# Kernel optimization log

Hardware: AMD Instinct MI355X
Metric: run time of the kernel (lower is better)

## Reference

```python
import jax, jax.numpy as jnp
import numpy as np

B, S, DIM = 2, 2048, 2048
H = 16
Q_RANK, KV_RANK = 512, 512
D_NOPE, D_ROPE, D_V = 128, 64, 128
D_QK = D_NOPE + D_ROPE  # 192
EPS = 1e-6
SCALE = D_QK ** -0.5


def setup_inputs() -> dict:
    key = jax.random.key(0)
    ks = jax.random.split(key, 8)
    x = jax.random.normal(ks[0], (B, S, DIM), dtype=jnp.float32)
    # real RoPE table: theta_i = 10000^{-2i/d}, angles = pos * theta
    inv_freq = 1.0 / (10000.0 ** (np.arange(0, D_ROPE, 2, dtype=np.float32) / D_ROPE))
    ang = np.arange(S, dtype=np.float32)[:, None] * inv_freq[None, :]  # (S, D_ROPE//2)
    freqs_cis = jnp.asarray(np.stack([np.cos(ang), np.sin(ang)], axis=-1))  # (S, 32, 2)
    std = 0.02
    wq_a = jax.random.normal(ks[1], (Q_RANK, DIM), dtype=jnp.float32) * std
    wq_b = jax.random.normal(ks[2], (H * D_QK, Q_RANK), dtype=jnp.float32) * std
    wkv_a = jax.random.normal(ks[3], (KV_RANK + D_ROPE, DIM), dtype=jnp.float32) * std
    wkv_b = jax.random.normal(ks[4], (H * (D_NOPE + D_V), KV_RANK), dtype=jnp.float32) * std
    wo = jax.random.normal(ks[5], (DIM, H * D_V), dtype=jnp.float32) * std
    q_norm_w = jnp.ones((Q_RANK,), dtype=jnp.float32)
    kv_norm_w = jnp.ones((KV_RANK,), dtype=jnp.float32)
    return {"x": x, "freqs_cis": freqs_cis, "wq_a": wq_a, "wq_b": wq_b,
            "q_norm_w": q_norm_w, "wkv_a": wkv_a, "kv_norm_w": kv_norm_w,
            "wkv_b": wkv_b, "wo": wo}


def _rmsnorm(x, w):
    var = jnp.mean(jnp.square(x), axis=-1, keepdims=True)
    return x * jax.lax.rsqrt(var + EPS) * w


def _rope(x, freqs_cis):
    # x: (B, S, h, d); freqs_cis: (S, d//2, 2) as (cos, sin). Pairs are interleaved (x0,x1),(x2,x3),...
    xr, xi = x[..., 0::2], x[..., 1::2]
    cos = freqs_cis[None, :, None, :, 0]
    sin = freqs_cis[None, :, None, :, 1]
    yr = xr * cos - xi * sin
    yi = xr * sin + xi * cos
    return jnp.stack([yr, yi], axis=-1).reshape(x.shape)


def reference(x, freqs_cis, wq_a, wq_b, q_norm_w, wkv_a, kv_norm_w, wkv_b, wo):
    b, s, _ = x.shape
    # low-rank Q projection: wq_a -> RMSNorm -> wq_b
    q = _rmsnorm(x @ wq_a.T, q_norm_w) @ wq_b.T
    q = q.reshape(b, s, H, D_QK)
    q_nope, q_pe = q[..., :D_NOPE], q[..., D_NOPE:]
    q = jnp.concatenate([q_nope, _rope(q_pe, freqs_cis)], axis=-1)  # (b,s,H,192)
    # KV path
    kv = x @ wkv_a.T  # (b,s,KV_RANK+D_ROPE)
    kv_lat, k_pe = kv[..., :KV_RANK], kv[..., KV_RANK:]
    k_pe = _rope(k_pe[:, :, None, :], freqs_cis)  # (b,s,1,64)
    kv = (_rmsnorm(kv_lat, kv_norm_w) @ wkv_b.T).reshape(b, s, H, D_NOPE + D_V)
    k_nope, v = kv[..., :D_NOPE], kv[..., D_NOPE:]
    k = jnp.concatenate([k_nope, jnp.broadcast_to(k_pe, (b, s, H, D_ROPE))], axis=-1)
    # causal scaled-dot-product attention
    scores = jnp.einsum('bshd,bthd->bhst', q, k) * SCALE
    mask = jnp.tril(jnp.ones((s, s), dtype=bool))
    scores = jnp.where(mask[None, None], scores, jnp.finfo(scores.dtype).min)
    probs = jax.nn.softmax(scores, axis=-1)
    out = jnp.einsum('bhst,bthd->bshd', probs, v).reshape(b, s, H * D_V)
    return out @ wo.T
```

## Files before the change

### kernel.cpp

```cpp
#include <hip/hip_runtime.h>
#include <cstdint>
#include <cstddef>


typedef unsigned short u16;
typedef unsigned int u32;
typedef unsigned long long u64;
typedef __attribute__((ext_vector_type(8))) short bf16x8;
typedef __attribute__((ext_vector_type(4))) float floatx4;

#define MFMA16x16x32 __builtin_amdgcn_mfma_f32_16x16x32_bf16

#define QSCALE 0.10411755f
#define THR_L2 11.541560f

__device__ __forceinline__ u16 f2bf(float f) {
  u32 u = __float_as_uint(f);
  u32 r = (u + 0x7fffu + ((u >> 16) & 1u)) >> 16;
  return (u16)r;
}
__device__ __forceinline__ float bf2f(u16 b) {
  return __uint_as_float(((u32)b) << 16);
}
__device__ __forceinline__ u32 cvtpk(float lo, float hi) {
  u32 r;
  asm("v_cvt_pk_bf16_f32 %0, %1, %2" : "=v"(r) : "v"(lo), "v"(hi));
  return r;
}
__device__ __forceinline__ void gload16(const void* g, void* l) {
  __builtin_amdgcn_global_load_lds(
      (const __attribute__((address_space(1))) void*)g,
      (__attribute__((address_space(3))) void*)l, 16, 0, 0);
}

__global__ __launch_bounds__(256) void cvt_all(
    const float* __restrict__ s0, const float* __restrict__ s1,
    const float* __restrict__ s2, const float* __restrict__ s3,
    const float* __restrict__ s4, const float* __restrict__ s5,
    u16* __restrict__ d0, u16* __restrict__ d1, u16* __restrict__ d2,
    u16* __restrict__ d3, u16* __restrict__ d4, u16* __restrict__ d5) {
  constexpr int ST1 = 2097152;
  constexpr int ST2 = ST1 + 262144;
  constexpr int ST3 = ST2 + 294912;
  constexpr int ST4 = ST3 + 393216;
  constexpr int ST5 = ST4 + 524288;
  constexpr int TOT = ST5 + 1048576;
  int i = blockIdx.x * 256 + threadIdx.x;
  int stride = gridDim.x * 256;
  for (; i < TOT; i += stride) {
    const float* sp;
    u16* dp;
    int j;
    if (i < ST1)      { sp = s0; dp = d0; j = i; }
    else if (i < ST2) { sp = s1; dp = d1; j = i - ST1; }
    else if (i < ST3) { sp = s2; dp = d2; j = i - ST2; }
    else if (i < ST4) { sp = s3; dp = d3; j = i - ST3; }
    else if (i < ST5) { sp = s4; dp = d4; j = i - ST4; }
    else              { sp = s5; dp = d5; j = i - ST5; }
    float4 v = ((const float4*)sp)[j];
    ushort4 o;
    o.x = f2bf(v.x); o.y = f2bf(v.y); o.z = f2bf(v.z); o.w = f2bf(v.w);
    ((ushort4*)dp)[j] = o;
  }
}

template <int BM, int BN, int EPI>
__global__ __launch_bounds__(512) void gemm8(const u16* __restrict__ A,
                                             const u16* __restrict__ B,
                                             void* __restrict__ Cv,
                                             int M, int N, int K,
                                             const float* __restrict__ fcp,
                                             void* __restrict__ aux) {
  constexpr int WM = BM / 2;
  constexpr int AF = WM / 16;
  constexpr int WN = BN / 4;
  constexpr int FN = WN / 16;
  constexpr int LA = BM * 4 / 512;
  constexpr int LB = BN * 4 / 512;
  constexpr int S = LA + LB;
  __shared__ alignas(16) u16 As[2][BM * 32];
  __shared__ alignas(16) u16 Bs[2][BN * 32];
  const int m0 = blockIdx.y * BM, n0 = blockIdx.x * BN;
  const int t = threadIdx.x;
  const int wv = t >> 6, lane = t & 63, g = lane >> 4, qq = lane & 15;
  const int wr = wv >> 2, wc = wv & 3;
  const int fsw = (qq >> 1) & 3;
  size_t aoff[LA], boff[LB];
#pragma unroll
  for (int i = 0; i < LA; ++i) {
    int seg = t + i * 512;
    int row = seg >> 2, sl = seg & 3;
    aoff[i] = (size_t)(m0 + row) * K + (sl ^ ((row >> 1) & 3)) * 8;
  }
#pragma unroll
  for (int i = 0; i < LB; ++i) {
    int seg = t + i * 512;
    int row = seg >> 2, sl = seg & 3;
    boff[i] = (size_t)(n0 + row) * K + (sl ^ ((row >> 1) & 3)) * 8;
  }
  const floatx4 fz = {0.f, 0.f, 0.f, 0.f};
  floatx4 acc[AF][FN];
#pragma unroll
  for (int m = 0; m < AF; ++m)
#pragma unroll
    for (int n = 0; n < FN; ++n) acc[m][n] = fz;

#define GS8(buf, k0)                                                          \
  {                                                                           \
    _Pragma("unroll") for (int i = 0; i < LA; ++i)                            \
        gload16(&A[aoff[i] + (k0)], &As[buf][(size_t)(wv * 64 + i * 512) * 8]); \
    _Pragma("unroll") for (int i = 0; i < LB; ++i)                            \
        gload16(&B[boff[i] + (k0)], &Bs[buf][(size_t)(wv * 64 + i * 512) * 8]); \
  }

  const int nk = K >> 5;
  GS8(0, 0);
  GS8(1, 32);
  for (int kt = 0; kt < nk; ++kt) {
    asm volatile("" ::: "memory");
    if (kt + 1 < nk) {
      if constexpr (S == 4)
        asm volatile("s_waitcnt vmcnt(4)" ::: "memory");
      else if constexpr (S == 3)
        asm volatile("s_waitcnt vmcnt(3)" ::: "memory");
      else
        asm volatile("s_waitcnt vmcnt(2)" ::: "memory");
    } else {
      asm volatile("s_waitcnt vmcnt(0)" ::: "memory");
    }
    __builtin_amdgcn_s_barrier();
    asm volatile("" ::: "memory");
    const u16* Ab = &As[kt & 1][0];
    const u16* Bb = &Bs[kt & 1][0];
    bf16x8 af[AF], bfr[FN];
#pragma unroll
    for (int m = 0; m < AF; ++m)
      af[m] = *(const bf16x8*)&Ab[(wr * WM + m * 16 + qq) * 32 + ((g ^ fsw) * 8)];
#pragma unroll
    for (int n = 0; n < FN; ++n)
      bfr[n] = *(const bf16x8*)&Bb[(wc * WN + n * 16 + qq) * 32 + ((g ^ fsw) * 8)];
    asm volatile("s_waitcnt lgkmcnt(0)" ::: "memory");
    __builtin_amdgcn_s_barrier();
    asm volatile("" ::: "memory");
    if (kt + 2 < nk) GS8(kt & 1, (kt + 2) * 32);
    __builtin_amdgcn_s_setprio(1);
#pragma unroll
    for (int m = 0; m < AF; ++m)
#pragma unroll
      for (int n = 0; n < FN; ++n)
        acc[m][n] = MFMA16x16x32(af[m], bfr[n], acc[m][n], 0, 0, 0);
    __builtin_amdgcn_s_setprio(0);
  }
#undef GS8

#pragma unroll
  for (int m = 0; m < AF; ++m)
#pragma unroll
    for (int n = 0; n < FN; ++n) {
      const int col16 = n0 + wc * WN + n * 16;
      if constexpr (EPI == 0 || EPI == 1) {
#pragma unroll
        for (int r = 0; r < 4; ++r) {
          int row = m0 + wr * WM + m * 16 + 4 * g + r;
          int col = col16 + qq;
          if constexpr (EPI == 1)
            ((u16*)Cv)[(size_t)row * N + col] = f2bf(acc[m][n][r]);
          else
            ((float*)Cv)[(size_t)row * N + col] = acc[m][n][r];
        }
      } else if constexpr (EPI == 2) {
        const int h = col16 / 192;
        const int jb = col16 - h * 192 + qq;
#pragma unroll
        for (int r = 0; r < 4; ++r) {
          int row = m0 + wr * WM + m * 16 + 4 * g + r;
          int b = row >> 11, s = row & 2047;
          float own = acc[m][n][r];
          float par = __shfl_xor(own, 1);
          if ((qq & 1) == 0) {
            u32 w;
            if (jb < 128) {
              w = cvtpk(own * QSCALE, par * QSCALE);
            } else {
              int jp = (jb - 128) >> 1;
              float c = fcp[(s * 32 + jp) * 2];
              float sn = fcp[(s * 32 + jp) * 2 + 1];
              w = cvtpk((own * c - par * sn) * QSCALE,
                        (own * sn + par * c) * QSCALE);
            }
            *(u32*)((u16*)Cv + ((size_t)(b * 16 + h) * 2048 + s) * 192 + jb) = w;
          }
        }
      } else {
        const int h = col16 >> 8;
        const int jb = (col16 & 255) + qq;
        if (jb < 128) {
#pragma unroll
          for (int r = 0; r < 4; ++r) {
            int row = m0 + wr * WM + m * 16 + 4 * g + r;
            int b = row >> 11, s = row & 2047;
            float own = acc[m][n][r];
            float par = __shfl_xor(own, 1);
            if ((qq & 1) == 0)
              *(u32*)((u16*)Cv + ((size_t)(b * 16 + h) * 2048 + s) * 192 + jb) =
                  cvtpk(own, par);
          }
        } else {
          int row0 = m0 + wr * WM + m * 16 + 4 * g;
          int b = row0 >> 11, s0v = row0 & 2047;
          int dv = jb - 128;
          u32 lo = cvtpk(acc[m][n][0], acc[m][n][1]);
          u32 hi = cvtpk(acc[m][n][2], acc[m][n][3]);
          u64 w = (u64)lo | ((u64)hi << 32);
          *(u64*)((u16*)aux + ((size_t)(b * 16 + h) * 128 + dv) * 2048 + s0v) = w;
        }
      }
    }
}

__global__ __launch_bounds__(256) void rmsnorm2(const u16* __restrict__ ap,
                                                const float* __restrict__ qw,
                                                const float* __restrict__ kw,
                                                u16* __restrict__ qout,
                                                u16* __restrict__ kout) {
  const int bid = blockIdx.x, t = threadIdx.x;
  const bool isq = bid < 4096;
  const int row = isq ? bid : bid - 4096;
  const u16* in = ap + (size_t)row * 1280 + (isq ? 0 : 512);
  const float* w = isq ? qw : kw;
  u16* out = (isq ? qout : kout) + (size_t)row * 512;
  __shared__ float wsum[4];
  u32 wv2 = *(const u32*)&in[2 * t];
  float vx = bf2f((u16)wv2), vy = bf2f((u16)(wv2 >> 16));
  float ss = vx * vx + vy * vy;
#pragma unroll
  for (int off = 1; off < 64; off <<= 1) ss += __shfl_xor(ss, off);
  if ((t & 63) == 0) wsum[t >> 6] = ss;
  __syncthreads();
  float tot = wsum[0] + wsum[1] + wsum[2] + wsum[3];
  float r = rsqrtf(tot * (1.f / 512.f) + 1e-6f);
  *(u32*)&out[2 * t] = cvtpk(vx * r * w[2 * t], vy * r * w[2 * t + 1]);
}

__global__ __launch_bounds__(256) void rope_kpe_bcast(const u16* __restrict__ ap,
                                                      const float* __restrict__ fc,
                                                      u16* __restrict__ kbf) {
  int idx = blockIdx.x * 256 + threadIdx.x;
  int row = idx >> 5, j = idx & 31;
  int b = row >> 11, s = row & 2047;
  u32 wv2 = *(const u32*)&ap[(size_t)row * 1280 + 1024 + 2 * j];
  float xr = bf2f((u16)wv2), xi = bf2f((u16)(wv2 >> 16));
  float c = fc[(s * 32 + j) * 2], sn = fc[(s * 32 + j) * 2 + 1];
  u32 w = cvtpk(xr * c - xi * sn, xr * sn + xi * c);
#pragma unroll
  for (int h = 0; h < 16; ++h)
    *(u32*)&kbf[((size_t)(b * 16 + h) * 2048 + s) * 192 + 128 + 2 * j] = w;
}

__global__ __launch_bounds__(256, 4) void flash_attn(const u16* __restrict__ Q,
                                                     const u16* __restrict__ Kc,
                                                     const u16* __restrict__ VT,
                                                     u16* __restrict__ O) {
  __shared__ alignas(16) u16 Ks[2][32 * 192];
  __shared__ alignas(16) u16 Vs[2][128 * 32];
  const int bid = blockIdx.x;
  const int qt = 31 - (bid >> 5);
  const int bh = bid & 31;
  const int t = threadIdx.x, wv = t >> 6, lane = t & 63;
  const int g = lane >> 4, qq = lane & 15;
  const int qrow0 = qt * 64 + wv * 16;
  const int my_last = qrow0 + 15;
  const int q_glob = qrow0 + qq;
  const int nkt = 2 * qt + 2;

  int koffg[3], voffg[2];
#pragma unroll
  for (int i = 0; i < 3; ++i) {
    int seg = t + i * 256;
    int row = seg / 24, sl = seg - row * 24;
    koffg[i] = row * 192 + (sl ^ ((row >> 1) & 7)) * 8;
  }
#pragma unroll
  for (int i = 0; i < 2; ++i) {
    int seg = t + i * 256;
    int row = seg >> 2, sl = seg & 3;
    voffg[i] = row * 2048 + (sl ^ ((row >> 1) & 3)) * 8;
  }
  const u16* Kt0 = Kc + (size_t)bh * 2048 * 192;
  const u16* Vt0 = VT + (size_t)bh * 128 * 2048;

  bf16x8 qf[6];
  {
    const u16* qp = Q + ((size_t)bh * 2048 + qrow0 + qq) * 192;
#pragma unroll
    for (int kk = 0; kk < 6; ++kk) qf[kk] = *(const bf16x8*)&qp[kk * 32 + g * 8];
  }
  asm volatile("s_waitcnt vmcnt(0)" ::: "memory");

  const floatx4 fz = {0.f, 0.f, 0.f, 0.f};
  floatx4 oacc[8];
  floatx4 oacc_l = fz;
#pragma unroll
  for (int d = 0; d < 8; ++d) oacc[d] = fz;
  float m_run = -1e30f;

  bf16x8 ones;
#pragma unroll
  for (int i = 0; i < 8; ++i) ones[i] = (short)0x3f80;

  const int krow0 = 2 * qq;
  const int krow1 = 2 * qq + 1;
  const int xrk = qq & 7;
  const int vsw = (qq >> 1) & 3;

#define STAGE(buf, kt)                                                       \
  {                                                                          \
    const u16* Kg = Kt0 + (size_t)(kt) * (32 * 192);                         \
    const u16* Vg = Vt0 + (kt) * 32;                                         \
    _Pragma("unroll") for (int i = 0; i < 3; ++i)                            \
        gload16(Kg + koffg[i], &Ks[buf][(size_t)(wv * 64 + i * 256) * 8]);   \
    _Pragma("unroll") for (int i = 0; i < 2; ++i)                            \
        gload16(Vg + voffg[i], &Vs[buf][(size_t)(wv * 64 + i * 256) * 8]);   \
  }

  STAGE(0, 0);
  for (int kt = 0; kt < nkt; ++kt) {
    const int k0 = kt * 32;
    asm volatile("" ::: "memory");
    if (kt + 1 < nkt) {
      STAGE((kt + 1) & 1, kt + 1);
      asm volatile("s_waitcnt vmcnt(5)" ::: "memory");
    } else {
      asm volatile("s_waitcnt vmcnt(0)" ::: "memory");
    }
    __builtin_amdgcn_s_barrier();
    asm volatile("" ::: "memory");
    if (k0 <= my_last) {
      const u16* Kb = &Ks[kt & 1][0];
      const u16* Vb = &Vs[kt & 1][0];
      floatx4 s0 = fz, s1 = fz;
      __builtin_amdgcn_s_setprio(1);
#pragma unroll
      for (int kk = 0; kk < 6; ++kk) {
        int sl = kk * 4 + g;
        bf16x8 a0 = *(const bf16x8*)&Kb[krow0 * 192 + ((sl ^ xrk) * 8)];
        bf16x8 a1 = *(const bf16x8*)&Kb[krow1 * 192 + ((sl ^ xrk) * 8)];
        s0 = MFMA16x16x32(a0, qf[kk], s0, 0, 0, 0);
        s1 = MFMA16x16x32(a1, qf[kk], s1, 0, 0, 0);
      }
      __builtin_amdgcn_s_setprio(0);
      float v[8];
      if (k0 + 31 <= qrow0) {
#pragma unroll
        for (int r = 0; r < 4; ++r) {
          v[r] = s0[r];
          v[4 + r] = s1[r];
        }
      } else {
#pragma unroll
        for (int r = 0; r < 4; ++r) {
          int key0 = k0 + 8 * g + 2 * r;
          v[r] = (key0 <= q_glob) ? s0[r] : -1e30f;
          v[4 + r] = (key0 + 1 <= q_glob) ? s1[r] : -1e30f;
        }
      }
      float mloc = fmaxf(fmaxf(fmaxf(v[0], v[1]), fmaxf(v[2], v[3])),
                         fmaxf(fmaxf(v[4], v[5]), fmaxf(v[6], v[7])));
      if (!__all(mloc <= m_run + THR_L2)) {
        float mx = fmaxf(mloc, __shfl_xor(mloc, 16));
        mx = fmaxf(mx, __shfl_xor(mx, 32));
        float m_new = fmaxf(m_run, mx);
        float alpha = exp2f(m_run - m_new);
        m_run = m_new;
#pragma unroll
        for (int d = 0; d < 8; ++d)
#pragma unroll
          for (int r = 0; r < 4; ++r) oacc[d][r] *= alpha;
#pragma unroll
        for (int r = 0; r < 4; ++r) oacc_l[r] *= alpha;
      }
      float pex[8];
#pragma unroll
      for (int i = 0; i < 8; ++i) pex[i] = exp2f(v[i] - m_run);
      bf16x8 pf;
      ((u32*)&pf)[0] = cvtpk(pex[0], pex[4]);
      ((u32*)&pf)[1] = cvtpk(pex[1], pex[5]);
      ((u32*)&pf)[2] = cvtpk(pex[2], pex[6]);
      ((u32*)&pf)[3] = cvtpk(pex[3], pex[7]);
      __builtin_amdgcn_s_setprio(1);
#pragma unroll
      for (int d = 0; d < 8; ++d) {
        bf16x8 vf = *(const bf16x8*)&Vb[(d * 16 + qq) * 32 + ((g ^ vsw) * 8)];
        oacc[d] = MFMA16x16x32(vf, pf, oacc[d], 0, 0, 0);
      }
      oacc_l = MFMA16x16x32(ones, pf, oacc_l, 0, 0, 0);
      __builtin_amdgcn_s_setprio(0);
    }
    asm volatile("" ::: "memory");
    __builtin_amdgcn_s_barrier();
  }
#undef STAGE
  float linv = 1.f / oacc_l[0];
  const int b = bh >> 4, h = bh & 15;
  size_t rowoff = ((size_t)b * 2048 + qrow0 + qq) * 2048 + h * 128 + 4 * g;
#pragma unroll
  for (int d = 0; d < 8; ++d) {
    u32 lo = cvtpk(oacc[d][0] * linv, oacc[d][1] * linv);
    u32 hi = cvtpk(oacc[d][2] * linv, oacc[d][3] * linv);
    u64 w = (u64)lo | ((u64)hi << 32);
    *(u64*)&O[rowoff + d * 16] = w;
  }
}

extern "C" void kernel_launch(void* const* d_in, const int* in_sizes, int n_in,
                              void* d_out, int out_size, void* d_ws,
                              size_t ws_size, hipStream_t stream) {
  (void)in_sizes; (void)n_in; (void)out_size;
  const float* x = (const float*)d_in[0];
  const float* fc = (const float*)d_in[1];
  const float* wqa = (const float*)d_in[2];
  const float* wqb = (const float*)d_in[3];
  const float* qnw = (const float*)d_in[4];
  const float* wkva = (const float*)d_in[5];
  const float* kvnw = (const float*)d_in[6];
  const float* wkvb = (const float*)d_in[7];
  const float* wo = (const float*)d_in[8];
  float* out = (float*)d_out;
  char* ws = (char*)d_ws;

  size_t off = 0;
  auto alloc = [&](size_t bytes) {
    size_t o = off;
    off += (bytes + 255) & ~(size_t)255;
    return o;
  };
  const size_t o_xbf = alloc(16777216);
  const size_t o_wa = alloc(5242880);
  const size_t o_wqb = alloc(3145728);
  const size_t o_wkvb = alloc(4194304);
  const size_t o_wo = alloc(8388608);
  const size_t o_qln = alloc(4194304);
  const size_t o_kvln = alloc(4194304);
  const size_t o_ap = alloc(10485760);
  const size_t o_qbf = alloc(25165824);
  const size_t o_kbf = alloc(25165824);
  const size_t o_vt = alloc(16777216);
  if (ws_size < off) return;

  u16* xbf = (u16*)(ws + o_xbf);
  u16* wab = (u16*)(ws + o_wa);
  u16* wqbb = (u16*)(ws + o_wqb);
  u16* wkvbb = (u16*)(ws + o_wkvb);
  u16* wob = (u16*)(ws + o_wo);
  u16* qlatn = (u16*)(ws + o_qln);
  u16* kvlatn = (u16*)(ws + o_kvln);
  u16* ap = (u16*)(ws + o_ap);
  u16* qbf = (u16*)(ws + o_qbf);
  u16* kbf = (u16*)(ws + o_kbf);
  u16* vt = (u16*)(ws + o_vt);
  u16* attnbf = (u16*)(ws + o_xbf);

  cvt_all<<<2048, 256, 0, stream>>>(x, wqa, wkva, wqb, wkvb, wo,
                                    xbf, wab, wab + 1048576, wqbb, wkvbb, wob);

  gemm8<128, 128, 1><<<dim3(10, 32), 512, 0, stream>>>(
      xbf, wab, ap, 4096, 1280, 2048, nullptr, nullptr);
  rmsnorm2<<<8192, 256, 0, stream>>>(ap, qnw, kvnw, qlatn, kvlatn);
  rope_kpe_bcast<<<512, 256, 0, stream>>>(ap, fc, kbf);

  gemm8<128, 256, 2><<<dim3(12, 32), 512, 0, stream>>>(
      qlatn, wqbb, qbf, 4096, 3072, 512, fc, nullptr);

  gemm8<128, 256, 3><<<dim3(16, 32), 512, 0, stream>>>(
      kvlatn, wkvbb, kbf, 4096, 4096, 512, nullptr, vt);

  flash_attn<<<1024, 256, 0, stream>>>(qbf, kbf, vt, attnbf);
  gemm8<128, 128, 0><<<dim3(16, 32), 512, 0, stream>>>(
      attnbf, wob, out, 4096, 2048, 2048, nullptr, nullptr);
}
```

Baseline: 246.5 us.

## Process two 16-row query groups per wave in flash attention

Each wave now handles 32 query rows (two 16-row groups), so every block covers 128 query rows and the grid is halved to 512 blocks. Each K/V fragment read from LDS feeds twice as many MFMAs, which raises compute per LDS byte and halves the total number of K/V tile loads. The cost is higher register pressure (double accumulators and Q fragments) under launch_bounds(256,4). Fewer blocks may also balance less evenly across the causal triangle and leave the GPU less occupied.

New measurement: 448.3 us. +81.9%, slower.

```diff
diff --git a/kernel.cpp b/kernel.cpp
--- a/kernel.cpp
+++ b/kernel.cpp
@@ -264,14 +264,13 @@
   __shared__ alignas(16) u16 Ks[2][32 * 192];
   __shared__ alignas(16) u16 Vs[2][128 * 32];
   const int bid = blockIdx.x;
-  const int qt = 31 - (bid >> 5);
+  const int qt = 15 - (bid >> 5);
   const int bh = bid & 31;
   const int t = threadIdx.x, wv = t >> 6, lane = t & 63;
   const int g = lane >> 4, qq = lane & 15;
-  const int qrow0 = qt * 64 + wv * 16;
-  const int my_last = qrow0 + 15;
-  const int q_glob = qrow0 + qq;
-  const int nkt = 2 * qt + 2;
+  const int qrow0 = qt * 128 + wv * 32;
+  const int my_last = qrow0 + 31;
+  const int nkt = 4 * qt + 4;
 
   int koffg[3], voffg[2];
 #pragma unroll
@@ -289,20 +288,24 @@
   const u16* Kt0 = Kc + (size_t)bh * 2048 * 192;
   const u16* Vt0 = VT + (size_t)bh * 128 * 2048;
 
-  bf16x8 qf[6];
-  {
-    const u16* qp = Q + ((size_t)bh * 2048 + qrow0 + qq) * 192;
-#pragma unroll
-    for (int kk = 0; kk < 6; ++kk) qf[kk] = *(const bf16x8*)&qp[kk * 32 + g * 8];
+  bf16x8 qf[2][6];
+#pragma unroll
+  for (int qg = 0; qg < 2; ++qg) {
+    const u16* qp = Q + ((size_t)bh * 2048 + qrow0 + qg * 16 + qq) * 192;
+#pragma unroll
+    for (int kk = 0; kk < 6; ++kk)
+      qf[qg][kk] = *(const bf16x8*)&qp[kk * 32 + g * 8];
   }
   asm volatile("s_waitcnt vmcnt(0)" ::: "memory");
 
   const floatx4 fz = {0.f, 0.f, 0.f, 0.f};
-  floatx4 oacc[8];
-  floatx4 oacc_l = fz;
-#pragma unroll
-  for (int d = 0; d < 8; ++d) oacc[d] = fz;
-  float m_run = -1e30f;
+  floatx4 oacc[2][8];
+  floatx4 oacc_l[2] = {fz, fz};
+#pragma unroll
+  for (int qg = 0; qg < 2; ++qg)
+#pragma unroll
+    for (int d = 0; d < 8; ++d) oacc[qg][d] = fz;
+  float m_run[2] = {-1e30f, -1e30f};
 
   bf16x8 ones;
 #pragma unroll
@@ -338,77 +341,89 @@
     if (k0 <= my_last) {
       const u16* Kb = &Ks[kt & 1][0];
       const u16* Vb = &Vs[kt & 1][0];
-      floatx4 s0 = fz, s1 = fz;
+      floatx4 s0[2] = {fz, fz}, s1[2] = {fz, fz};
       __builtin_amdgcn_s_setprio(1);
 #pragma unroll
       for (int kk = 0; kk < 6; ++kk) {
         int sl = kk * 4 + g;
         bf16x8 a0 = *(const bf16x8*)&Kb[krow0 * 192 + ((sl ^ xrk) * 8)];
         bf16x8 a1 = *(const bf16x8*)&Kb[krow1 * 192 + ((sl ^ xrk) * 8)];
-        s0 = MFMA16x16x32(a0, qf[kk], s0, 0, 0, 0);
-        s1 = MFMA16x16x32(a1, qf[kk], s1, 0, 0, 0);
+        s0[0] = MFMA16x16x32(a0, qf[0][kk], s0[0], 0, 0, 0);
+        s1[0] = MFMA16x16x32(a1, qf[0][kk], s1[0], 0, 0, 0);
+        s0[1] = MFMA16x16x32(a0, qf[1][kk], s0[1], 0, 0, 0);
+        s1[1] = MFMA16x16x32(a1, qf[1][kk], s1[1], 0, 0, 0);
       }
       __builtin_amdgcn_s_setprio(0);
-      float v[8];
-      if (k0 + 31 <= qrow0) {
-#pragma unroll
-        for (int r = 0; r < 4; ++r) {
-          v[r] = s0[r];
-          v[4 + r] = s1[r];
+      bf16x8 pf[2];
+#pragma unroll
+      for (int qg = 0; qg < 2; ++qg) {
+        const int q_glob = qrow0 + qg * 16 + qq;
+        float v[8];
+        if (k0 + 31 <= qrow0 + qg * 16) {
+#pragma unroll
+          for (int r = 0; r < 4; ++r) {
+            v[r] = s0[qg][r];
+            v[4 + r] = s1[qg][r];
+          }
+        } else {
+#pragma unroll
+          for (int r = 0; r < 4; ++r) {
+            int key0 = k0 + 8 * g + 2 * r;
+            v[r] = (key0 <= q_glob) ? s0[qg][r] : -1e30f;
+            v[4 + r] = (key0 + 1 <= q_glob) ? s1[qg][r] : -1e30f;
+          }
         }
-      } else {
-#pragma unroll
-        for (int r = 0; r < 4; ++r) {
-          int key0 = k0 + 8 * g + 2 * r;
-          v[r] = (key0 <= q_glob) ? s0[r] : -1e30f;
-          v[4 + r] = (key0 + 1 <= q_glob) ? s1[r] : -1e30f;
+        float mloc = fmaxf(fmaxf(fmaxf(v[0], v[1]), fmaxf(v[2], v[3])),
+                           fmaxf(fmaxf(v[4], v[5]), fmaxf(v[6], v[7])));
+        if (!__all(mloc <= m_run[qg] + THR_L2)) {
+          float mx = fmaxf(mloc, __shfl_xor(mloc, 16));
+          mx = fmaxf(mx, __shfl_xor(mx, 32));
+          float m_new = fmaxf(m_run[qg], mx);
+          float alpha = exp2f(m_run[qg] - m_new);
+          m_run[qg] = m_new;
+#pragma unroll
+          for (int d = 0; d < 8; ++d)
+#pragma unroll
+            for (int r = 0; r < 4; ++r) oacc[qg][d][r] *= alpha;
+#pragma unroll
+          for (int r = 0; r < 4; ++r) oacc_l[qg][r] *= alpha;
         }
+        float pex[8];
+#pragma unroll
+        for (int i = 0; i < 8; ++i) pex[i] = exp2f(v[i] - m_run[qg]);
+        ((u32*)&pf[qg])[0] = cvtpk(pex[0], pex[4]);
+        ((u32*)&pf[qg])[1] = cvtpk(pex[1], pex[5]);
+        ((u32*)&pf[qg])[2] = cvtpk(pex[2], pex[6]);
+        ((u32*)&pf[qg])[3] = cvtpk(pex[3], pex[7]);
       }
-      float mloc = fmaxf(fmaxf(fmaxf(v[0], v[1]), fmaxf(v[2], v[3])),
-                         fmaxf(fmaxf(v[4], v[5]), fmaxf(v[6], v[7])));
-      if (!__all(mloc <= m_run + THR_L2)) {
-        float mx = fmaxf(mloc, __shfl_xor(mloc, 16));
-        mx = fmaxf(mx, __shfl_xor(mx, 32));
-        float m_new = fmaxf(m_run, mx);
-        float alpha = exp2f(m_run - m_new);
-        m_run = m_new;
-#pragma unroll
-        for (int d = 0; d < 8; ++d)
-#pragma unroll
-          for (int r = 0; r < 4; ++r) oacc[d][r] *= alpha;
-#pragma unroll
-        for (int r = 0; r < 4; ++r) oacc_l[r] *= alpha;
-      }
-      float pex[8];
-#pragma unroll
-      for (int i = 0; i < 8; ++i) pex[i] = exp2f(v[i] - m_run);
-      bf16x8 pf;
-      ((u32*)&pf)[0] = cvtpk(pex[0], pex[4]);
-      ((u32*)&pf)[1] = cvtpk(pex[1], pex[5]);
-      ((u32*)&pf)[2] = cvtpk(pex[2], pex[6]);
-      ((u32*)&pf)[3] = cvtpk(pex[3], pex[7]);
       __builtin_amdgcn_s_setprio(1);
 #pragma unroll
       for (int d = 0; d < 8; ++d) {
         bf16x8 vf = *(const bf16x8*)&Vb[(d * 16 + qq) * 32 + ((g ^ vsw) * 8)];
-        oacc[d] = MFMA16x16x32(vf, pf, oacc[d], 0, 0, 0);
+        oacc[0][d] = MFMA16x16x32(vf, pf[0], oacc[0][d], 0, 0, 0);
+        oacc[1][d] = MFMA16x16x32(vf, pf[1], oacc[1][d], 0, 0, 0);
       }
-      oacc_l = MFMA16x16x32(ones, pf, oacc_l, 0, 0, 0);
+      oacc_l[0] = MFMA16x16x32(ones, pf[0], oacc_l[0], 0, 0, 0);
+      oacc_l[1] = MFMA16x16x32(ones, pf[1], oacc_l[1], 0, 0, 0);
       __builtin_amdgcn_s_setprio(0);
     }
     asm volatile("" ::: "memory");
     __builtin_amdgcn_s_barrier();
   }
 #undef STAGE
-  float linv = 1.f / oacc_l[0];
   const int b = bh >> 4, h = bh & 15;
-  size_t rowoff = ((size_t)b * 2048 + qrow0 + qq) * 2048 + h * 128 + 4 * g;
-#pragma unroll
-  for (int d = 0; d < 8; ++d) {
-    u32 lo = cvtpk(oacc[d][0] * linv, oacc[d][1] * linv);
-    u32 hi = cvtpk(oacc[d][2] * linv, oacc[d][3] * linv);
-    u64 w = (u64)lo | ((u64)hi << 32);
-    *(u64*)&O[rowoff + d * 16] = w;
+#pragma unroll
+  for (int qg = 0; qg < 2; ++qg) {
+    float linv = 1.f / oacc_l[qg][0];
+    size_t rowoff =
+        ((size_t)b * 2048 + qrow0 + qg * 16 + qq) * 2048 + h * 128 + 4 * g;
+#pragma unroll
+    for (int d = 0; d < 8; ++d) {
+      u32 lo = cvtpk(oacc[qg][d][0] * linv, oacc[qg][d][1] * linv);
+      u32 hi = cvtpk(oacc[qg][d][2] * linv, oacc[qg][d][3] * linv);
+      u64 w = (u64)lo | ((u64)hi << 32);
+      *(u64*)&O[rowoff + d * 16] = w;
+    }
   }
 }
 
@@ -474,7 +489,7 @@
   gemm8<128, 256, 3><<<dim3(16, 32), 512, 0, stream>>>(
       kvlatn, wkvbb, kbf, 4096, 4096, 512, nullptr, vt);
 
-  flash_attn<<<1024, 256, 0, stream>>>(qbf, kbf, vt, attnbf);
+  flash_attn<<<512, 256, 0, stream>>>(qbf, kbf, vt, attnbf);
   gemm8<128, 128, 0><<<dim3(16, 32), 512, 0, stream>>>(
       attnbf, wob, out, 4096, 2048, 2048, nullptr, nullptr);
 }
```
